# Kernel optimization log

Measured on AMD Instinct MI355X. Metric: run time of the kernel, lower is better.

Reference implementation:

```python
import jax, jax.numpy as jnp
import numpy as np

N = 50000
E = 800000
IN_DIM = 128
HID = 32
HEADS = 8
OUT_DIM = 64
BN_EPS = 1e-5
NEG_SLOPE = 0.2


def batch_norm(x, gamma, beta, mean, var):
    # eval-mode BatchNorm1d using running statistics
    return (x - mean) * jax.lax.rsqrt(var + BN_EPS) * gamma + beta


def gat_conv(x, src, dst, W, att_src, att_dst, heads, out_ch, n):
    """PyG GATConv (shared src/dst lin), self-loops already included in src/dst.
    x: [n, in]; W: [in, heads*out_ch]; att_*: [heads, out_ch].
    Returns [n, heads, out_ch]."""
    h = (x @ W).reshape(n, heads, out_ch)                       # node features per head
    a_s = jnp.einsum('nho,ho->nh', h, att_src)                  # [n, heads]
    a_d = jnp.einsum('nho,ho->nh', h, att_dst)
    e = jax.nn.leaky_relu(a_s[src] + a_d[dst], NEG_SLOPE)       # [e, heads]
    # segment softmax over incoming edges of each dst node
    mx = jax.ops.segment_max(e, dst, num_segments=n)
    ex = jnp.exp(e - mx[dst])
    denom = jax.ops.segment_sum(ex, dst, num_segments=n)
    alpha = ex / (denom[dst] + 1e-16)                           # [e, heads]
    out = jax.ops.segment_sum(alpha[:, :, None] * h[src], dst, num_segments=n)
    return out                                                  # [n, heads, out_ch]


def setup_inputs() -> dict:
    key = jax.random.key(0)
    ks = jax.random.split(key, 24)
    inp = {}
    inp['x'] = jax.random.normal(ks[0], (N, IN_DIM), dtype=jnp.float32)
    inp['edge_index'] = jax.random.randint(ks[1], (2, E), 0, N, dtype=jnp.int64)
    s = 0.05
    inp['W1'] = jax.random.normal(ks[2], (IN_DIM, HEADS * HID), dtype=jnp.float32) * s
    inp['a_src1'] = jax.random.normal(ks[3], (HEADS, HID), dtype=jnp.float32) * s
    inp['a_dst1'] = jax.random.normal(ks[4], (HEADS, HID), dtype=jnp.float32) * s
    inp['b1'] = jnp.zeros((HEADS * HID,), dtype=jnp.float32)
    inp['W2'] = jax.random.normal(ks[5], (HEADS * HID, OUT_DIM), dtype=jnp.float32) * s
    inp['a_src2'] = jax.random.normal(ks[6], (1, OUT_DIM), dtype=jnp.float32) * s
    inp['a_dst2'] = jax.random.normal(ks[7], (1, OUT_DIM), dtype=jnp.float32) * s
    inp['b2'] = jnp.zeros((OUT_DIM,), dtype=jnp.float32)
    # projection Linear(out_dim -> in_dim)
    inp['Wp'] = jax.random.normal(ks[8], (OUT_DIM, IN_DIM), dtype=jnp.float32) * s
    inp['bp'] = jnp.zeros((IN_DIM,), dtype=jnp.float32)
    # BatchNorm params (eval mode running stats)
    for i, d in [(1, HEADS * HID), (2, OUT_DIM), (3, IN_DIM)]:
        k0, k1, k2, k3 = jax.random.split(ks[8 + i], 4)
        inp[f'g{i}'] = 1.0 + 0.1 * jax.random.normal(k0, (d,), dtype=jnp.float32)
        inp[f'be{i}'] = 0.1 * jax.random.normal(k1, (d,), dtype=jnp.float32)
        inp[f'm{i}'] = 0.1 * jax.random.normal(k2, (d,), dtype=jnp.float32)
        inp[f'v{i}'] = jax.random.uniform(k3, (d,), dtype=jnp.float32, minval=0.5, maxval=1.5)
    return inp


def reference(x, edge_index, W1, a_src1, a_dst1, b1, W2, a_src2, a_dst2, b2,
              Wp, bp, g1, be1, m1, v1, g2, be2, m2, v2, g3, be3, m3, v3):
    n = x.shape[0]
    loops = jnp.arange(n, dtype=edge_index.dtype)
    src = jnp.concatenate([edge_index[0], loops])   # add_self_loops=True (PyG default)
    dst = jnp.concatenate([edge_index[1], loops])

    h = gat_conv(x, src, dst, W1, a_src1, a_dst1, HEADS, HID, n)
    h = h.reshape(n, HEADS * HID) + b1              # concat=True
    h = jax.nn.elu(batch_norm(h, g1, be1, m1, v1))  # dropout is no-op in eval

    h = gat_conv(h, src, dst, W2, a_src2, a_dst2, 1, OUT_DIM, n)
    h = h.reshape(n, OUT_DIM) + b2                  # concat=False, heads=1 -> mean == identity
    h = jax.nn.elu(batch_norm(h, g2, be2, m2, v2))

    h = h @ Wp + bp
    return batch_norm(h, g3, be3, m3, v3)
```

## Files before the change

### kernel.cpp

```cpp
#include <hip/hip_runtime.h>
#include <math.h>

#define NEG_SLOPE 0.2f
#define BN_EPS 1e-5f

typedef __bf16 bf16x8 __attribute__((ext_vector_type(8)));
typedef float  f32x4  __attribute__((ext_vector_type(4)));

__device__ __forceinline__ float elu_f(float x){ return x > 0.f ? x : expm1f(x); }
__device__ __forceinline__ float lrelu_f(float x){ return x > 0.f ? x : NEG_SLOPE * x; }

__device__ __forceinline__ float b2f(ushort u){
    union { uint i; float f; } v; v.i = (uint)u << 16; return v.f;
}
__device__ __forceinline__ ushort f2b(float f){
    union { float f; uint i; } v; v.f = f;
    uint r = v.i + 0x7FFFu + ((v.i >> 16) & 1u);
    return (ushort)(r >> 16);
}

__device__ __forceinline__ bool detect_f64(const void* ei, int E, long long N)
{
    const long long* p = (const long long*)ei;
    int lane = threadIdx.x & 63;
    long long v = p[lane % max(1, min(2 * E, 64))];
    bool bad = (v < 0 || v >= N);
    return __ballot(bad) == 0ull;
}

__device__ __forceinline__ void get_edge(const void* ei, int e, int E, bool f64, int& s, int& d)
{
    if (e < E) {
        if (f64) { const long long* p = (const long long*)ei; s = (int)p[e]; d = (int)p[E + e]; }
        else     { const int*       p = (const int*)ei;       s = p[e];      d = p[E + e]; }
    } else {
        s = d = e - E;
    }
}

__global__ void setup_kernel(const void* ei, int E, int N, int* deg, int cx,
    const float* __restrict__ x, ushort* __restrict__ xb,
    const float* __restrict__ W1, const float* __restrict__ W2, const float* __restrict__ Wp,
    ushort* __restrict__ wt1, ushort* __restrict__ wt2, ushort* __restrict__ wtp,
    const float* b1, const float* b2, const float* bp,
    const float* g1, const float* be1, const float* m1, const float* v1,
    const float* g2, const float* be2, const float* m2, const float* v2,
    const float* g3, const float* be3, const float* m3, const float* v3,
    float* par)
{
    int b = blockIdx.x, t = threadIdx.x;
    if (b == 0) {
        { float s = g1[t] * rsqrtf(v1[t] + BN_EPS); par[t] = s;        par[256 + t] = b1[t] * s + be1[t] - m1[t] * s; }
        if (t < 64)  { float s = g2[t] * rsqrtf(v2[t] + BN_EPS); par[512 + t] = s;  par[576 + t] = b2[t] * s + be2[t] - m2[t] * s; }
        if (t < 128) { float s = g3[t] * rsqrtf(v3[t] + BN_EPS); par[640 + t] = s;  par[768 + t] = bp[t] * s + be3[t] - m3[t] * s; }
    } else if (b <= 224) {
        int idx = (b - 1) * 256 + t;
        if (idx < 32768) {
            int n = idx >> 7, k = idx & 127;
            wt1[idx] = f2b(W1[k * 256 + n]);
        } else if (idx < 49152) {
            int j = idx - 32768;
            int n = j >> 8, k = j & 255;
            wt2[j] = f2b(W2[k * 64 + n]);
        } else if (idx < 57344) {
            int j = idx - 49152;
            int n = j >> 6, k = j & 63;
            wtp[j] = f2b(Wp[k * 128 + n]);
        }
    } else if (b < 225 + cx) {
        long long n128 = (long long)N * 128;
        long long idx = ((long long)(b - 225) * 256 + t) * 8;
        if (idx + 7 < n128) {
            float4 v0 = *reinterpret_cast<const float4*>(&x[idx]);
            float4 v1 = *reinterpret_cast<const float4*>(&x[idx + 4]);
            ushort o[8] = { f2b(v0.x), f2b(v0.y), f2b(v0.z), f2b(v0.w),
                            f2b(v1.x), f2b(v1.y), f2b(v1.z), f2b(v1.w) };
            uint4 pk;
            pk.x = (uint)o[0] | ((uint)o[1] << 16);
            pk.y = (uint)o[2] | ((uint)o[3] << 16);
            pk.z = (uint)o[4] | ((uint)o[5] << 16);
            pk.w = (uint)o[6] | ((uint)o[7] << 16);
            *reinterpret_cast<uint4*>(&xb[idx]) = pk;
        } else {
            for (long long q = idx; q < n128; ++q) xb[q] = f2b(x[q]);
        }
    } else {
        bool f64 = detect_f64(ei, E, (long long)N);
        int i = (b - 225 - cx) * 256 + t;
        int ET = E + N;
        if (i < ET) {
            int s, d;
            get_edge(ei, i, E, f64, s, d);
            atomicAdd(&deg[d], 1);
        }
    }
}

__global__ void scan1_kernel(const int* __restrict__ deg, int N, int* __restrict__ bsum)
{
    int b = blockIdx.x, t = threadIdx.x;
    int base = b * 4096 + t * 16;
    int s = 0;
    #pragma unroll
    for (int k = 0; k < 16; k += 4) {
        int idx = base + k;
        if (idx + 3 < N) {
            int4 v = *reinterpret_cast<const int4*>(&deg[idx]);
            s += v.x + v.y + v.z + v.w;
        } else {
            for (int q = 0; q < 4; ++q) if (idx + q < N) s += deg[idx + q];
        }
    }
    #pragma unroll
    for (int off = 1; off < 64; off <<= 1) s += __shfl_xor(s, off);
    __shared__ int wsum[4];
    if ((t & 63) == 0) wsum[t >> 6] = s;
    __syncthreads();
    if (t == 0) bsum[b] = wsum[0] + wsum[1] + wsum[2] + wsum[3];
}

__global__ void scan2_kernel(const int* __restrict__ bsum, int nb, int* __restrict__ bpre)
{
    if (threadIdx.x == 0) {
        int r = 0;
        for (int i = 0; i < nb; ++i) { bpre[i] = r; r += bsum[i]; }
        bpre[nb] = r;
    }
}

__global__ void scan3_kernel(const int* __restrict__ deg, int N,
                             const int* __restrict__ bpre, int nb,
                             int* __restrict__ rowptr, int* __restrict__ fillptr)
{
    int b = blockIdx.x, t = threadIdx.x;
    int base = b * 4096 + t * 16;
    int loc[16];
    int s = 0;
    #pragma unroll
    for (int k = 0; k < 16; ++k) {
        int idx = base + k;
        int d = (idx < N) ? deg[idx] : 0;
        loc[k] = s; s += d;
    }
    int lane = t & 63;
    int incl = s;
    #pragma unroll
    for (int off = 1; off < 64; off <<= 1) {
        int v = __shfl_up(incl, off);
        if (lane >= off) incl += v;
    }
    __shared__ int wsum[4];
    if (lane == 63) wsum[t >> 6] = incl;
    __syncthreads();
    int woff = 0;
    int w = t >> 6;
    for (int i = 0; i < w; ++i) woff += wsum[i];
    int off0 = bpre[b] + woff + incl - s;
    #pragma unroll
    for (int k = 0; k < 16; ++k) {
        int idx = base + k;
        if (idx < N) { rowptr[idx] = off0 + loc[k]; fillptr[idx] = off0 + loc[k]; }
    }
    if (b == 0 && t == 0) rowptr[N] = bpre[nb];
}

__global__ void fill_kernel(const void* ei, int E, int N, int* fillptr, int* esrc)
{
    bool f64 = detect_f64(ei, E, (long long)N);
    int i = blockIdx.x * blockDim.x + threadIdx.x;
    int ET = E + N;
    if (i >= ET) return;
    int s, d;
    get_edge(ei, i, E, f64, s, d);
    int pos = atomicAdd(&fillptr[d], 1);
    esrc[pos] = s;
}

template<int ATYPE, int OMODE, int ATT>
__global__ __launch_bounds__(256) void mgemm_kernel(const void* __restrict__ Ap,
    const ushort* __restrict__ Bt, void* __restrict__ Cp, int M, int K, int NC,
    const float* __restrict__ S, const float* __restrict__ Cc,
    const float* __restrict__ att_s, const float* __restrict__ att_d,
    float* __restrict__ as_out, float* __restrict__ ad_out)
{
    const int BM = 128, LDA = 72;
    __shared__ __align__(16) ushort As[BM][LDA];
    __shared__ __align__(16) ushort Bs[64][LDA];
    __shared__ float red[128][2];
    int t = threadIdx.x;
    int m0 = blockIdx.x * BM, n0 = blockIdx.y * 64;
    int w = t >> 6, l = t & 63;
    int wm = w >> 1, wn = w & 1;
    int r16 = l & 15, kg = l >> 4;

    f32x4 acc[4][2];
    #pragma unroll
    for (int mi = 0; mi < 4; ++mi)
        #pragma unroll
        for (int ni = 0; ni < 2; ++ni)
            acc[mi][ni] = (f32x4){0.f, 0.f, 0.f, 0.f};

    for (int kb = 0; kb < K; kb += 64) {
        if (ATYPE == 0) {
            const float* A = (const float*)Ap;
            #pragma unroll
            for (int p = 0; p < 8; ++p) {
                int r = (t >> 4) + p * 16, c4 = (t & 15) * 4;
                int gm = m0 + r;
                float4 v = (gm < M) ? *reinterpret_cast<const float4*>(&A[(size_t)gm * K + kb + c4])
                                    : make_float4(0.f, 0.f, 0.f, 0.f);
                ushort4 u; u.x = f2b(v.x); u.y = f2b(v.y); u.z = f2b(v.z); u.w = f2b(v.w);
                *reinterpret_cast<ushort4*>(&As[r][c4]) = u;
            }
        } else {
            const ushort* A = (const ushort*)Ap;
            #pragma unroll
            for (int p = 0; p < 4; ++p) {
                int r = (t >> 3) + p * 32, c8 = (t & 7) * 8;
                int gm = m0 + r;
                uint4 v = (gm < M) ? *reinterpret_cast<const uint4*>(&A[(size_t)gm * K + kb + c8])
                                   : make_uint4(0u, 0u, 0u, 0u);
                *reinterpret_cast<uint4*>(&As[r][c8]) = v;
            }
        }
        #pragma unroll
        for (int p = 0; p < 2; ++p) {
            int r = (t >> 3) + p * 32, c8 = (t & 7) * 8;
            uint4 v = *reinterpret_cast<const uint4*>(&Bt[(size_t)(n0 + r) * K + kb + c8]);
            *reinterpret_cast<uint4*>(&Bs[r][c8]) = v;
        }
        __syncthreads();
        #pragma unroll
        for (int kk = 0; kk < 2; ++kk) {
            bf16x8 bB[2], bA[4];
            #pragma unroll
            for (int ni = 0; ni < 2; ++ni)
                bB[ni] = *reinterpret_cast<const bf16x8*>(&Bs[wn * 32 + ni * 16 + r16][kk * 32 + kg * 8]);
            #pragma unroll
            for (int mi = 0; mi < 4; ++mi)
                bA[mi] = *reinterpret_cast<const bf16x8*>(&As[wm * 64 + mi * 16 + r16][kk * 32 + kg * 8]);
            #pragma unroll
            for (int mi = 0; mi < 4; ++mi)
                #pragma unroll
                for (int ni = 0; ni < 2; ++ni)
                    acc[mi][ni] = __builtin_amdgcn_mfma_f32_16x16x32_bf16(bA[mi], bB[ni], acc[mi][ni], 0, 0, 0);
        }
        __syncthreads();
    }
    #pragma unroll
    for (int mi = 0; mi < 4; ++mi) {
        #pragma unroll
        for (int ni = 0; ni < 2; ++ni) {
            #pragma unroll
            for (int rg = 0; rg < 4; ++rg) {
                int gm = m0 + wm * 64 + mi * 16 + kg * 4 + rg;
                int gc = n0 + wn * 32 + ni * 16 + r16;
                if (gm < M) {
                    float v = acc[mi][ni][rg];
                    if (OMODE == 0) {
                        size_t idx = (ATT == 1)
                            ? ((size_t)(gc >> 5) * M + gm) * 32 + (gc & 31)
                            : (size_t)gm * NC + gc;
                        ((ushort*)Cp)[idx] = f2b(v);
                    } else {
                        ((float*)Cp)[(size_t)gm * NC + gc] = v * S[gc] + Cc[gc];
                    }
                }
            }
        }
    }
    if (ATT) {
        float cs0 = att_s[n0 + wn * 32 + r16], cs1 = att_s[n0 + wn * 32 + 16 + r16];
        float cd0 = att_d[n0 + wn * 32 + r16], cd1 = att_d[n0 + wn * 32 + 16 + r16];
        float sp[4][4], dp[4][4];
        #pragma unroll
        for (int mi = 0; mi < 4; ++mi)
            #pragma unroll
            for (int rg = 0; rg < 4; ++rg) {
                sp[mi][rg] = acc[mi][0][rg] * cs0 + acc[mi][1][rg] * cs1;
                dp[mi][rg] = acc[mi][0][rg] * cd0 + acc[mi][1][rg] * cd1;
            }
        #pragma unroll
        for (int off = 1; off < 16; off <<= 1)
            #pragma unroll
            for (int mi = 0; mi < 4; ++mi)
                #pragma unroll
                for (int rg = 0; rg < 4; ++rg) {
                    sp[mi][rg] += __shfl_xor(sp[mi][rg], off);
                    dp[mi][rg] += __shfl_xor(dp[mi][rg], off);
                }
        if (ATT == 1) {
            int head = (n0 >> 5) + wn;
            if (r16 == 0) {
                #pragma unroll
                for (int mi = 0; mi < 4; ++mi)
                    #pragma unroll
                    for (int rg = 0; rg < 4; ++rg) {
                        int gm = m0 + wm * 64 + mi * 16 + kg * 4 + rg;
                        if (gm < M) {
                            as_out[(size_t)head * M + gm] = sp[mi][rg];
                            ad_out[(size_t)head * M + gm] = dp[mi][rg];
                        }
                    }
            }
        } else {
            if (wn == 1 && r16 == 0) {
                #pragma unroll
                for (int mi = 0; mi < 4; ++mi)
                    #pragma unroll
                    for (int rg = 0; rg < 4; ++rg) {
                        int r = wm * 64 + mi * 16 + kg * 4 + rg;
                        red[r][0] = sp[mi][rg];
                        red[r][1] = dp[mi][rg];
                    }
            }
            __syncthreads();
            if (wn == 0 && r16 == 0) {
                #pragma unroll
                for (int mi = 0; mi < 4; ++mi)
                    #pragma unroll
                    for (int rg = 0; rg < 4; ++rg) {
                        int r = wm * 64 + mi * 16 + kg * 4 + rg;
                        int gm = m0 + r;
                        if (gm < M) {
                            as_out[gm] = sp[mi][rg] + red[r][0];
                            ad_out[gm] = dp[mi][rg] + red[r][1];
                        }
                    }
            }
        }
    }
}

__global__ void agg1_kernel(const ushort* __restrict__ h1s,
                            const float* __restrict__ as1t, const float* __restrict__ ad1t,
                            const int* __restrict__ rowptr, const int* __restrict__ esrc,
                            const float* __restrict__ par,
                            ushort* __restrict__ outb, int N)
{
    __shared__ uint2 wslds[16][16];
    int s = blockIdx.x & 7;
    int wslot = threadIdx.x >> 6;
    int lane = threadIdx.x & 63;
    int q = lane >> 4, li = lane & 15;
    int row = wslot * 4 + q;
    int n = (blockIdx.x >> 3) * 16 + row;
    bool active = (n < N);
    int beg = 0, end = 0;
    float adv = 0.f;
    if (active) {
        beg = rowptr[n];
        end = rowptr[n + 1];
        adv = ad1t[(size_t)s * N + n];
    }
    const char* slabc = (const char*)(h1s + (size_t)s * N * 32);
    const float* as_s = as1t + (size_t)s * N;
    int sub = (lane >> 3) & 1;
    uint eoff = (uint)(lane & 7) * 8u;
    float den = 0.f;
    float acc[4] = {0.f, 0.f, 0.f, 0.f};

    for (int cb = beg; cb < end; cb += 16) {
        int cnt = min(16, end - cb);
        int cnt2 = (cnt + 1) & ~1;
        {
            float wv = 0.f;
            int src = n;
            if (li < cnt) {
                src = esrc[cb + li];
                wv = __expf(lrelu_f(as_s[src] + adv));
                den += wv;
            }
            if (li < cnt2) wslds[row][li] = make_uint2(__float_as_uint(wv), (uint)src);
        }
        __builtin_amdgcn_wave_barrier();
        auto fma4 = [&](uint2 r, float wgt) {
            union { uint u; float f; } c;
            c.u = r.x << 16;         acc[0] += wgt * c.f;
            c.u = r.x & 0xffff0000u; acc[1] += wgt * c.f;
            c.u = r.y << 16;         acc[2] += wgt * c.f;
            c.u = r.y & 0xffff0000u; acc[3] += wgt * c.f;
        };
        int kk = 0;
        for (; kk + 3 < cnt2; kk += 4) {
            uint2 ws0 = wslds[row][kk + sub];
            uint2 ws1 = wslds[row][kk + 2 + sub];
            uint2 r0 = *reinterpret_cast<const uint2*>(slabc + (ws0.y * 64u + eoff));
            uint2 r1 = *reinterpret_cast<const uint2*>(slabc + (ws1.y * 64u + eoff));
            fma4(r0, __uint_as_float(ws0.x));
            fma4(r1, __uint_as_float(ws1.x));
        }
        for (; kk < cnt2; kk += 2) {
            uint2 ws0 = wslds[row][kk + sub];
            uint2 r0 = *reinterpret_cast<const uint2*>(slabc + (ws0.y * 64u + eoff));
            fma4(r0, __uint_as_float(ws0.x));
        }
        __builtin_amdgcn_wave_barrier();
    }

    den += __shfl_xor(den, 1, 64);
    den += __shfl_xor(den, 2, 64);
    den += __shfl_xor(den, 4, 64);
    den += __shfl_xor(den, 8, 64);
    #pragma unroll
    for (int f = 0; f < 4; ++f) acc[f] += __shfl_xor(acc[f], 8, 64);
    if (active && sub == 0) {
        float inv = 1.f / (den + 1e-16f);
        int f = s * 32 + (lane & 7) * 4;
        float4 S1 = *reinterpret_cast<const float4*>(&par[f]);
        float4 C1 = *reinterpret_cast<const float4*>(&par[256 + f]);
        ushort4 o;
        o.x = f2b(elu_f(acc[0] * inv * S1.x + C1.x));
        o.y = f2b(elu_f(acc[1] * inv * S1.y + C1.y));
        o.z = f2b(elu_f(acc[2] * inv * S1.z + C1.z));
        o.w = f2b(elu_f(acc[3] * inv * S1.w + C1.w));
        *reinterpret_cast<ushort4*>(&outb[(size_t)n * 256 + f]) = o;
    }
}

__global__ void agg2_kernel(const ushort* __restrict__ h2,
                            const float* __restrict__ as2, const float* __restrict__ ad2,
                            const int* __restrict__ rowptr, const int* __restrict__ esrc,
                            const float* __restrict__ par,
                            ushort* __restrict__ outb, int N)
{
    __shared__ uint2 wslds_all[4][64];
    uint2* wlds = wslds_all[threadIdx.x >> 6];
    int wid = (blockIdx.x * blockDim.x + threadIdx.x) >> 6;
    int lane = threadIdx.x & 63;
    if (wid >= N) return;
    int beg = rowptr[wid], end = rowptr[wid + 1];
    int q = lane >> 4, li = lane & 15;
    uint foff = (uint)li * 8u;
    const char* h2c = (const char*)h2;
    float ad = ad2[wid];
    float den = 0.f;
    float acc[4] = {0.f, 0.f, 0.f, 0.f};

    for (int cb = beg; cb < end; cb += 64) {
        int cnt = min(64, end - cb);
        int cnt4 = (cnt + 3) & ~3;
        {
            float wv = 0.f;
            int src = wid;
            if (lane < cnt) {
                src = esrc[cb + lane];
                wv = __expf(lrelu_f(as2[src] + ad));
                den += wv;
            }
            if (lane < cnt4) wlds[lane] = make_uint2(__float_as_uint(wv), (uint)src);
        }
        __builtin_amdgcn_wave_barrier();
        auto fma4 = [&](uint2 r, float wgt) {
            union { uint u; float f; } c;
            c.u = r.x << 16;         acc[0] += wgt * c.f;
            c.u = r.x & 0xffff0000u; acc[1] += wgt * c.f;
            c.u = r.y << 16;         acc[2] += wgt * c.f;
            c.u = r.y & 0xffff0000u; acc[3] += wgt * c.f;
        };
        int k = q;
        for (; k + 7 < cnt4; k += 8) {
            uint2 ws0 = wlds[k];
            uint2 ws1 = wlds[k + 4];
            uint2 r0 = *reinterpret_cast<const uint2*>(h2c + (ws0.y * 128u + foff));
            uint2 r1 = *reinterpret_cast<const uint2*>(h2c + (ws1.y * 128u + foff));
            fma4(r0, __uint_as_float(ws0.x));
            fma4(r1, __uint_as_float(ws1.x));
        }
        for (; k < cnt4; k += 4) {
            uint2 ws0 = wlds[k];
            uint2 r0 = *reinterpret_cast<const uint2*>(h2c + (ws0.y * 128u + foff));
            fma4(r0, __uint_as_float(ws0.x));
        }
        __builtin_amdgcn_wave_barrier();
    }

    #pragma unroll
    for (int off = 1; off < 64; off <<= 1) den += __shfl_xor(den, off, 64);
    float inv = 1.f / (den + 1e-16f);
    #pragma unroll
    for (int f = 0; f < 4; ++f) {
        acc[f] += __shfl_xor(acc[f], 16, 64);
        acc[f] += __shfl_xor(acc[f], 32, 64);
    }
    if (lane < 16) {
        int f = li * 4;
        float4 S2 = *reinterpret_cast<const float4*>(&par[512 + f]);
        float4 C2 = *reinterpret_cast<const float4*>(&par[576 + f]);
        ushort4 o;
        o.x = f2b(elu_f(acc[0] * inv * S2.x + C2.x));
        o.y = f2b(elu_f(acc[1] * inv * S2.y + C2.y));
        o.z = f2b(elu_f(acc[2] * inv * S2.z + C2.z));
        o.w = f2b(elu_f(acc[3] * inv * S2.w + C2.w));
        *reinterpret_cast<ushort4*>(&outb[(size_t)wid * 64 + f]) = o;
    }
}

extern "C" void kernel_launch(void* const* d_in, const int* in_sizes, int n_in,
                              void* d_out, int out_size, void* d_ws, size_t ws_size,
                              hipStream_t stream)
{
    const float* x      = (const float*)d_in[0];
    const void*  ei     = d_in[1];
    const float* W1     = (const float*)d_in[2];
    const float* a_src1 = (const float*)d_in[3];
    const float* a_dst1 = (const float*)d_in[4];
    const float* b1     = (const float*)d_in[5];
    const float* W2     = (const float*)d_in[6];
    const float* a_src2 = (const float*)d_in[7];
    const float* a_dst2 = (const float*)d_in[8];
    const float* b2     = (const float*)d_in[9];
    const float* Wp     = (const float*)d_in[10];
    const float* bp     = (const float*)d_in[11];
    const float* g1 = (const float*)d_in[12], *be1 = (const float*)d_in[13];
    const float* m1 = (const float*)d_in[14], *v1  = (const float*)d_in[15];
    const float* g2 = (const float*)d_in[16], *be2 = (const float*)d_in[17];
    const float* m2 = (const float*)d_in[18], *v2  = (const float*)d_in[19];
    const float* g3 = (const float*)d_in[20], *be3 = (const float*)d_in[21];
    const float* m3 = (const float*)d_in[22], *v3  = (const float*)d_in[23];
    float* out = (float*)d_out;

    const int N  = in_sizes[0] / 128;
    const int E  = in_sizes[1] / 2;
    const int ET = E + N;

    char* base = (char*)d_ws;
    size_t off = 0;
    auto alloc = [&](size_t bytes) -> char* {
        char* p = base + off;
        off += (bytes + 255) & ~(size_t)255;
        return p;
    };
    float*  par     = (float*)alloc(1024 * 4);
    int*    bsum    = (int*)alloc(256);
    int*    bpre    = (int*)alloc(256);
    int*    rowptr  = (int*)alloc((size_t)(N + 1) * 4);
    int*    fillptr = (int*)alloc((size_t)(N + 1) * 4);
    int*    esrc    = (int*)alloc((size_t)ET * 4);
    float*  as1     = (float*)alloc((size_t)N * 8 * 4);
    float*  ad1     = (float*)alloc((size_t)N * 8 * 4);
    float*  as2     = (float*)alloc((size_t)N * 4);
    float*  ad2     = (float*)alloc((size_t)N * 4);
    ushort* wt1     = (ushort*)alloc(256 * 128 * 2);
    ushort* wt2     = (ushort*)alloc(64 * 256 * 2);
    ushort* wtp     = (ushort*)alloc(128 * 64 * 2);
    ushort* xb      = (ushort*)alloc((size_t)N * 128 * 2);
    ushort* h1      = (ushort*)alloc((size_t)N * 256 * 2);
    ushort* h1b     = (ushort*)alloc((size_t)N * 256 * 2);
    ushort* h2      = (ushort*)alloc((size_t)N * 64 * 2);
    ushort* g2buf   = (ushort*)alloc((size_t)N * 64 * 2);

    hipMemsetAsync(fillptr, 0, (N + 1) * sizeof(int), stream);
    int cx = (int)(((size_t)N * 128 + 2047) / 2048);
    int cblocks = (ET + 255) / 256;
    setup_kernel<<<225 + cx + cblocks, 256, 0, stream>>>(ei, E, N, fillptr, cx,
        x, xb, W1, W2, Wp, wt1, wt2, wtp,
        b1, b2, bp, g1, be1, m1, v1, g2, be2, m2, v2, g3, be3, m3, v3, par);

    int nb = (N + 4095) / 4096;
    scan1_kernel<<<nb, 256, 0, stream>>>(fillptr, N, bsum);
    scan2_kernel<<<1, 64, 0, stream>>>(bsum, nb, bpre);
    scan3_kernel<<<nb, 256, 0, stream>>>(fillptr, N, bpre, nb, rowptr, fillptr);
    fill_kernel<<<cblocks, 256, 0, stream>>>(ei, E, N, fillptr, esrc);

    int mb128 = (N + 127) / 128;
    int wbl   = (N + 3) / 4;
    mgemm_kernel<1, 0, 1><<<dim3(mb128, 4), 256, 0, stream>>>(xb, wt1, h1, N, 128, 256,
        nullptr, nullptr, a_src1, a_dst1, as1, ad1);
    int a1blocks = ((N + 15) / 16) * 8;
    agg1_kernel<<<a1blocks, 256, 0, stream>>>(h1, as1, ad1, rowptr, esrc, par, h1b, N);

    mgemm_kernel<1, 0, 2><<<dim3(mb128, 1), 256, 0, stream>>>(h1b, wt2, h2, N, 256, 64,
        nullptr, nullptr, a_src2, a_dst2, as2, ad2);
    agg2_kernel<<<wbl, 256, 0, stream>>>(h2, as2, ad2, rowptr, esrc, par, g2buf, N);

    mgemm_kernel<1, 1, 0><<<dim3(mb128, 2), 256, 0, stream>>>(g2buf, wtp, out, N, 64, 128,
        par + 640, par + 768, nullptr, nullptr, nullptr, nullptr);
}
```

Baseline: 289.5 us.

## Unify GAT aggregation kernels with head-sliced layout and cache-warming prefill

```diff
diff --git a/kernel.cpp b/kernel.cpp
--- a/kernel.cpp
+++ b/kernel.cpp
@@ -176,6 +176,25 @@
     esrc[pos] = s;
 }
 
+__global__ void prefill_kernel(const char* __restrict__ base, int N, int NS)
+{
+    int k = blockIdx.x & 7;
+    int s = k & (NS - 1);
+    int g = blockIdx.x >> 3;
+    int ngrp = gridDim.x >> 3;
+    size_t slab = (size_t)N * 64;
+    size_t per = (slab + ngrp - 1) / ngrp;
+    size_t b0 = (size_t)g * per;
+    size_t b1 = b0 + per; if (b1 > slab) b1 = slab;
+    const char* p = base + (size_t)s * slab;
+    uint acc = 0;
+    for (size_t o = b0 + (size_t)threadIdx.x * 16; o < b1; o += (size_t)blockDim.x * 16) {
+        uint4 v = *reinterpret_cast<const uint4*>(p + o);
+        acc ^= v.x ^ v.y ^ v.z ^ v.w;
+    }
+    asm volatile("" :: "v"(acc));
+}
+
 template<int ATYPE, int OMODE, int ATT>
 __global__ __launch_bounds__(256) void mgemm_kernel(const void* __restrict__ Ap,
     const ushort* __restrict__ Bt, void* __restrict__ Cp, int M, int K, int NC,
@@ -258,7 +277,7 @@
                 if (gm < M) {
                     float v = acc[mi][ni][rg];
                     if (OMODE == 0) {
-                        size_t idx = (ATT == 1)
+                        size_t idx = (ATT >= 1)
                             ? ((size_t)(gc >> 5) * M + gm) * 32 + (gc & 31)
                             : (size_t)gm * NC + gc;
                         ((ushort*)Cp)[idx] = f2b(v);
@@ -332,47 +351,46 @@
     }
 }
 
-__global__ void agg1_kernel(const ushort* __restrict__ h1s,
-                            const float* __restrict__ as1t, const float* __restrict__ ad1t,
-                            const int* __restrict__ rowptr, const int* __restrict__ esrc,
-                            const float* __restrict__ par,
-                            ushort* __restrict__ outb, int N)
-{
-    __shared__ uint2 wslds[16][16];
-    int s = blockIdx.x & 7;
+template<int NS, bool SATT>
+__global__ void agg_kernel(const ushort* __restrict__ hs,
+                           const float* __restrict__ ast, const float* __restrict__ adt,
+                           const int* __restrict__ rowptr, const int* __restrict__ esrc,
+                           const float* __restrict__ Sv, const float* __restrict__ Cv,
+                           ushort* __restrict__ outb, int N)
+{
+    const int CH = 64;
+    __shared__ uint2 wslds[16][CH];
+    int s = blockIdx.x & (NS - 1);
     int wslot = threadIdx.x >> 6;
     int lane = threadIdx.x & 63;
-    int q = lane >> 4, li = lane & 15;
-    int row = wslot * 4 + q;
-    int n = (blockIdx.x >> 3) * 16 + row;
+    int qq = lane >> 4, li = lane & 15;
+    int row = wslot * 4 + qq;
+    int n = (int)(blockIdx.x / NS) * 16 + row;
     bool active = (n < N);
     int beg = 0, end = 0;
     float adv = 0.f;
     if (active) {
         beg = rowptr[n];
         end = rowptr[n + 1];
-        adv = ad1t[(size_t)s * N + n];
-    }
-    const char* slabc = (const char*)(h1s + (size_t)s * N * 32);
-    const float* as_s = as1t + (size_t)s * N;
+        adv = SATT ? adt[(size_t)s * N + n] : adt[n];
+    }
+    const float* as_s = SATT ? (ast + (size_t)s * N) : ast;
+    const char* slabc = (const char*)(hs + (size_t)s * N * 32);
     int sub = (lane >> 3) & 1;
     uint eoff = (uint)(lane & 7) * 8u;
     float den = 0.f;
     float acc[4] = {0.f, 0.f, 0.f, 0.f};
 
-    for (int cb = beg; cb < end; cb += 16) {
-        int cnt = min(16, end - cb);
+    for (int cb = beg; cb < end; cb += CH) {
+        int cnt = min(CH, end - cb);
         int cnt2 = (cnt + 1) & ~1;
-        {
-            float wv = 0.f;
-            int src = n;
-            if (li < cnt) {
-                src = esrc[cb + li];
-                wv = __expf(lrelu_f(as_s[src] + adv));
-                den += wv;
-            }
-            if (li < cnt2) wslds[row][li] = make_uint2(__float_as_uint(wv), (uint)src);
-        }
+        for (int i = li; i < cnt; i += 16) {
+            int src = esrc[cb + i];
+            float wv = __expf(lrelu_f(as_s[src] + adv));
+            wslds[row][i] = make_uint2(__float_as_uint(wv), (uint)src);
+            den += wv;
+        }
+        if (li == 0 && (cnt & 1)) wslds[row][cnt] = make_uint2(0u, (uint)n);
         __builtin_amdgcn_wave_barrier();
         auto fma4 = [&](uint2 r, float wgt) {
             union { uint u; float f; } c;
@@ -407,92 +425,14 @@
     if (active && sub == 0) {
         float inv = 1.f / (den + 1e-16f);
         int f = s * 32 + (lane & 7) * 4;
-        float4 S1 = *reinterpret_cast<const float4*>(&par[f]);
-        float4 C1 = *reinterpret_cast<const float4*>(&par[256 + f]);
+        float4 Sc = *reinterpret_cast<const float4*>(&Sv[f]);
+        float4 Cc = *reinterpret_cast<const float4*>(&Cv[f]);
         ushort4 o;
-        o.x = f2b(elu_f(acc[0] * inv * S1.x + C1.x));
-        o.y = f2b(elu_f(acc[1] * inv * S1.y + C1.y));
-        o.z = f2b(elu_f(acc[2] * inv * S1.z + C1.z));
-        o.w = f2b(elu_f(acc[3] * inv * S1.w + C1.w));
-        *reinterpret_cast<ushort4*>(&outb[(size_t)n * 256 + f]) = o;
-    }
-}
-
-__global__ void agg2_kernel(const ushort* __restrict__ h2,
-                            const float* __restrict__ as2, const float* __restrict__ ad2,
-                            const int* __restrict__ rowptr, const int* __restrict__ esrc,
-                            const float* __restrict__ par,
-                            ushort* __restrict__ outb, int N)
-{
-    __shared__ uint2 wslds_all[4][64];
-    uint2* wlds = wslds_all[threadIdx.x >> 6];
-    int wid = (blockIdx.x * blockDim.x + threadIdx.x) >> 6;
-    int lane = threadIdx.x & 63;
-    if (wid >= N) return;
-    int beg = rowptr[wid], end = rowptr[wid + 1];
-    int q = lane >> 4, li = lane & 15;
-    uint foff = (uint)li * 8u;
-    const char* h2c = (const char*)h2;
-    float ad = ad2[wid];
-    float den = 0.f;
-    float acc[4] = {0.f, 0.f, 0.f, 0.f};
-
-    for (int cb = beg; cb < end; cb += 64) {
-        int cnt = min(64, end - cb);
-        int cnt4 = (cnt + 3) & ~3;
-        {
-            float wv = 0.f;
-            int src = wid;
-            if (lane < cnt) {
-                src = esrc[cb + lane];
-                wv = __expf(lrelu_f(as2[src] + ad));
-                den += wv;
-            }
-            if (lane < cnt4) wlds[lane] = make_uint2(__float_as_uint(wv), (uint)src);
-        }
-        __builtin_amdgcn_wave_barrier();
-        auto fma4 = [&](uint2 r, float wgt) {
-            union { uint u; float f; } c;
-            c.u = r.x << 16;         acc[0] += wgt * c.f;
-            c.u = r.x & 0xffff0000u; acc[1] += wgt * c.f;
-            c.u = r.y << 16;         acc[2] += wgt * c.f;
-            c.u = r.y & 0xffff0000u; acc[3] += wgt * c.f;
-        };
-        int k = q;
-        for (; k + 7 < cnt4; k += 8) {
-            uint2 ws0 = wlds[k];
-            uint2 ws1 = wlds[k + 4];
-            uint2 r0 = *reinterpret_cast<const uint2*>(h2c + (ws0.y * 128u + foff));
-            uint2 r1 = *reinterpret_cast<const uint2*>(h2c + (ws1.y * 128u + foff));
-            fma4(r0, __uint_as_float(ws0.x));
-            fma4(r1, __uint_as_float(ws1.x));
-        }
-        for (; k < cnt4; k += 4) {
-            uint2 ws0 = wlds[k];
-            uint2 r0 = *reinterpret_cast<const uint2*>(h2c + (ws0.y * 128u + foff));
-            fma4(r0, __uint_as_float(ws0.x));
-        }
-        __builtin_amdgcn_wave_barrier();
-    }
-
-    #pragma unroll
-    for (int off = 1; off < 64; off <<= 1) den += __shfl_xor(den, off, 64);
-    float inv = 1.f / (den + 1e-16f);
-    #pragma unroll
-    for (int f = 0; f < 4; ++f) {
-        acc[f] += __shfl_xor(acc[f], 16, 64);
-        acc[f] += __shfl_xor(acc[f], 32, 64);
-    }
-    if (lane < 16) {
-        int f = li * 4;
-        float4 S2 = *reinterpret_cast<const float4*>(&par[512 + f]);
-        float4 C2 = *reinterpret_cast<const float4*>(&par[576 + f]);
-        ushort4 o;
-        o.x = f2b(elu_f(acc[0] * inv * S2.x + C2.x));
-        o.y = f2b(elu_f(acc[1] * inv * S2.y + C2.y));
-        o.z = f2b(elu_f(acc[2] * inv * S2.z + C2.z));
-        o.w = f2b(elu_f(acc[3] * inv * S2.w + C2.w));
-        *reinterpret_cast<ushort4*>(&outb[(size_t)wid * 64 + f]) = o;
+        o.x = f2b(elu_f(acc[0] * inv * Sc.x + Cc.x));
+        o.y = f2b(elu_f(acc[1] * inv * Sc.y + Cc.y));
+        o.z = f2b(elu_f(acc[2] * inv * Sc.z + Cc.z));
+        o.w = f2b(elu_f(acc[3] * inv * Sc.w + Cc.w));
+        *reinterpret_cast<ushort4*>(&outb[(size_t)n * (NS * 32) + f]) = o;
     }
 }
 
@@ -564,15 +504,18 @@
     fill_kernel<<<cblocks, 256, 0, stream>>>(ei, E, N, fillptr, esrc);
 
     int mb128 = (N + 127) / 128;
-    int wbl   = (N + 3) / 4;
+    int ngrp16 = (N + 15) / 16;
     mgemm_kernel<1, 0, 1><<<dim3(mb128, 4), 256, 0, stream>>>(xb, wt1, h1, N, 128, 256,
         nullptr, nullptr, a_src1, a_dst1, as1, ad1);
-    int a1blocks = ((N + 15) / 16) * 8;
-    agg1_kernel<<<a1blocks, 256, 0, stream>>>(h1, as1, ad1, rowptr, esrc, par, h1b, N);
+    prefill_kernel<<<512, 256, 0, stream>>>((const char*)h1, N, 8);
+    agg_kernel<8, true><<<ngrp16 * 8, 256, 0, stream>>>(h1, as1, ad1, rowptr, esrc,
+        par, par + 256, h1b, N);
 
     mgemm_kernel<1, 0, 2><<<dim3(mb128, 1), 256, 0, stream>>>(h1b, wt2, h2, N, 256, 64,
         nullptr, nullptr, a_src2, a_dst2, as2, ad2);
-    agg2_kernel<<<wbl, 256, 0, stream>>>(h2, as2, ad2, rowptr, esrc, par, g2buf, N);
+    prefill_kernel<<<512, 256, 0, stream>>>((const char*)h2, N, 2);
+    agg_kernel<2, false><<<ngrp16 * 2, 256, 0, stream>>>(h2, as2, ad2, rowptr, esrc,
+        par + 512, par + 576, g2buf, N);
 
     mgemm_kernel<1, 1, 0><<<dim3(mb128, 2), 256, 0, stream>>>(g2buf, wtp, out, N, 64, 128,
         par + 640, par + 768, nullptr, nullptr, nullptr, nullptr);
```

Result: no change. 291.9 us (+0.8%).
